# Performance work log

Hardware: AMD Instinct MI355X
Metric: run time of the kernel (lower is better)

## Reference

```python
import jax, jax.numpy as jnp
import numpy as np

B = 8
INPUT_SHAPE = (32, 32, 32)
N = int(np.prod(INPUT_SHAPE))  # 32768
K = 128


def setup_inputs() -> dict:
    key = jax.random.key(0)
    k1, k2, k3, k4 = jax.random.split(key, 4)
    data = jax.random.normal(k1, (B,) + INPUT_SHAPE, dtype=jnp.float32)
    mask = jax.random.uniform(k2, (B,) + INPUT_SHAPE, dtype=jnp.float32)
    mult = jax.random.normal(k3, (N, K), dtype=jnp.float32) * 0.05  # RandomNormal init
    sigma_sq = jax.random.normal(k4, (1,), dtype=jnp.float32) * 0.05
    return {"data": data, "mask": mask, "mult": mult, "sigma_sq": sigma_sq}


def reference(data, mask, mult, sigma_sq):
    # Two-arg branch of SpatiallySparseDense_old.call (a_fact == 1).
    b = data.shape[0]
    n, k = mult.shape
    data_flat = data.reshape(b, n)          # [B, N]
    mask_flat = mask.reshape(b, n)          # [B, N]
    # W0 = mask_flat * mult, per batch: [B, N, K]
    W0 = mask_flat[:, :, None] * mult[None, :, :]
    # Gram matrix W0^T W0 + sigma^2 * I : [B, K, K]
    gram = jnp.einsum('bnk,bnl->bkl', W0, W0)
    seye = sigma_sq[0] * jnp.eye(k, dtype=data.dtype)
    pre = jnp.linalg.inv(gram + seye[None])  # [B, K, K] (matches tf.linalg.inv)
    # m = W0^T data : [B, K, 1]
    m = jnp.einsum('bnk,bn->bk', W0, data_flat)[..., None]
    res = jnp.matmul(pre, m)                # [B, K, 1]
    return res
```

## Files before the change

### kernel.cpp

```cpp
#include <hip/hip_runtime.h>

#define BATCH 8
#define NN 32768
#define KK 128
#define NCHUNK 32
#define CHUNK 1024
#define NST 16
#define NITER 8

typedef __attribute__((ext_vector_type(8)))  _Float16 half8;
typedef __attribute__((ext_vector_type(4)))  _Float16 half4;
typedef __attribute__((ext_vector_type(16))) float    f32x16;

#define MT_OFF   0ull
#define WH_OFF   (MT_OFF + 8388608ull)
#define DH_OFF   (WH_OFF + 524288ull)
#define GP_OFF   (DH_OFF + 524288ull)
#define MP_OFF   (GP_OFF + 5242880ull)
#define G_OFF    (MP_OFF + 131072ull)

__global__ __launch_bounds__(256) void prep_kernel(
    const float* __restrict__ data, const float* __restrict__ mask,
    const float* __restrict__ mult, unsigned char* __restrict__ ws)
{
    __shared__ _Float16 t[128][136];
    const int tid = threadIdx.x;
    const int n0  = blockIdx.x * 128;

    {
        const int b = tid >> 5, q = tid & 31;
        const size_t src = (size_t)b * NN + n0 + q * 4;
        const float4 d4 = *(const float4*)(data + src);
        const float4 m4 = *(const float4*)(mask + src);
        half4 w = { (_Float16)m4.x, (_Float16)m4.y, (_Float16)m4.z, (_Float16)m4.w };
        half4 d = { (_Float16)d4.x, (_Float16)d4.y, (_Float16)d4.z, (_Float16)d4.w };
        *(half4*)((_Float16*)(ws + WH_OFF) + src) = w;
        *(half4*)((_Float16*)(ws + DH_OFF) + src) = d;
    }

    const float4* m4p = (const float4*)mult;
#pragma unroll
    for (int u = 0; u < 16; ++u) {
        const int c16 = u * 256 + tid;
        const int n  = c16 >> 5;
        const int kq = c16 & 31;
        float4 v = m4p[(size_t)(n0 + n) * 32 + kq];
        half4 h = { (_Float16)v.x, (_Float16)v.y, (_Float16)v.z, (_Float16)v.w };
        const int c4s = kq ^ ((n >> 3) & 7);
        *(half4*)&t[n][c4s * 4] = h;
    }
    __syncthreads();

    _Float16* mt = (_Float16*)(ws + MT_OFF);
    const int g = tid & 15;
#pragma unroll
    for (int i = 0; i < 8; ++i) {
        const int k = (tid >> 4) + i * 16;
        const int c4 = (k >> 2) ^ 7;
        half8 v;
#pragma unroll
        for (int j = 0; j < 8; ++j) {
            const int n = g * 8 + j;
            const int cs = (k >> 2) ^ ((n >> 3) & 7);
            v[j] = t[n][cs * 4 + (k & 3)];
        }
        (void)c4;
        *(half8*)(mt + (size_t)k * NN + n0 + g * 8) = v;
    }
}

__global__ __launch_bounds__(256, 1) void gram_kernel(
    unsigned char* __restrict__ ws)
{
    __shared__ unsigned char smem[36864];
    const int tid = threadIdx.x;
    const int b     = blockIdx.x >> 5;
    const int chunk = blockIdx.x & 31;
    const int n0    = chunk * CHUNK;
    const int w = tid >> 6, l = tid & 63;

    const _Float16* mt = (const _Float16*)(ws + MT_OFF);

    if (tid < 128) {
        half8 wv = *(const half8*)((const _Float16*)(ws + WH_OFF) + (size_t)b * NN + n0 + tid * 8);
        half8 dv = *(const half8*)((const _Float16*)(ws + DH_OFF) + (size_t)b * NN + n0 + tid * 8);
        *(half8*)(smem + 32768 + tid * 16) = wv;
        *(half8*)(smem + 34816 + tid * 16) = dv;
    }

    const int krow = tid >> 3;
    const int gd   = tid & 7;
    const _Float16* gsrc0 = mt + (size_t)krow * NN + n0 + gd * 8;
    const int wslot = (gd ^ (krow & 7)) * 16;

    uint4 S0, S1, S2, S3;
#define GLOAD(st_) { const _Float16* p = gsrc0 + (size_t)(st_) * 64;          \
        S0 = *(const uint4*)(p);                                              \
        S1 = *(const uint4*)(p + (size_t)32 * NN);                            \
        S2 = *(const uint4*)(p + (size_t)64 * NN);                            \
        S3 = *(const uint4*)(p + (size_t)96 * NN); }
#define DSWRITE(buf_) { unsigned char* bp = smem + (buf_) * 16384 + krow * 128 + wslot; \
        *(uint4*)(bp)         = S0;  *(uint4*)(bp + 4096)  = S1;              \
        *(uint4*)(bp + 8192)  = S2;  *(uint4*)(bp + 12288) = S3; }

    const int frow  = (l & 31) * 128;
    const int fslot = ((w * 2 + (l >> 5)) ^ (l & 7)) * 16;
    const int wdoff = w * 32 + (l >> 5) * 16;

    f32x16 a00 = {}, a01 = {}, a02 = {}, a03 = {}, a11 = {},
           a12 = {}, a13 = {}, a22 = {}, a23 = {}, a33 = {};
    float macc0 = 0.f, macc1 = 0.f, macc2 = 0.f, macc3 = 0.f;

    GLOAD(0);
    __syncthreads();
    DSWRITE(0);
    GLOAD(1);
    __syncthreads();

#pragma unroll 2
    for (int st = 0; st < NST; ++st) {
        const int cur = st & 1;
        if (st < NST - 1) {
            DSWRITE(cur ^ 1);
            if (st < NST - 2) GLOAD(st + 2);
        }
        const unsigned char* tb = smem + cur * 16384;
        const half8 wf = *(const half8*)(smem + 32768 + st * 128 + wdoff);
        const half8 df = *(const half8*)(smem + 34816 + st * 128 + wdoff);
        half8 f0 = *(const half8*)(tb +     0 + frow + fslot) * wf;
        half8 f1 = *(const half8*)(tb +  4096 + frow + fslot) * wf;
        half8 f2 = *(const half8*)(tb +  8192 + frow + fslot) * wf;
        half8 f3 = *(const half8*)(tb + 12288 + frow + fslot) * wf;
#pragma unroll
        for (int j = 0; j < 8; ++j) {
            const float dj = (float)df[j];
            macc0 = fmaf((float)f0[j], dj, macc0);
            macc1 = fmaf((float)f1[j], dj, macc1);
            macc2 = fmaf((float)f2[j], dj, macc2);
            macc3 = fmaf((float)f3[j], dj, macc3);
        }
        a00 = __builtin_amdgcn_mfma_f32_32x32x16_f16(f0, f0, a00, 0, 0, 0);
        a01 = __builtin_amdgcn_mfma_f32_32x32x16_f16(f0, f1, a01, 0, 0, 0);
        a02 = __builtin_amdgcn_mfma_f32_32x32x16_f16(f0, f2, a02, 0, 0, 0);
        a03 = __builtin_amdgcn_mfma_f32_32x32x16_f16(f0, f3, a03, 0, 0, 0);
        a11 = __builtin_amdgcn_mfma_f32_32x32x16_f16(f1, f1, a11, 0, 0, 0);
        a12 = __builtin_amdgcn_mfma_f32_32x32x16_f16(f1, f2, a12, 0, 0, 0);
        a13 = __builtin_amdgcn_mfma_f32_32x32x16_f16(f1, f3, a13, 0, 0, 0);
        a22 = __builtin_amdgcn_mfma_f32_32x32x16_f16(f2, f2, a22, 0, 0, 0);
        a23 = __builtin_amdgcn_mfma_f32_32x32x16_f16(f2, f3, a23, 0, 0, 0);
        a33 = __builtin_amdgcn_mfma_f32_32x32x16_f16(f3, f3, a33, 0, 0, 0);
        __syncthreads();
    }

    {
        float* M = (float*)(smem + 32768);
        const int base = (w * 2 + (l >> 5)) * 128 + (l & 31);
        M[base +  0] = macc0;  M[base + 32] = macc1;
        M[base + 64] = macc2;  M[base + 96] = macc3;
    }
    _Float16* Gp = (_Float16*)(ws + GP_OFF) + (size_t)(b * NCHUNK + chunk) * 10240;
    float* Mp = (float*)(ws + MP_OFF) + (size_t)(b * NCHUNK + chunk) * KK;
    float* R = (float*)smem;

#define PHASE(p_, A0_, A1_)                                                    \
    {                                                                          \
        *(f32x16*)(R + (w * 2 + 0) * 1024 + l * 16) = A0_;                     \
        *(f32x16*)(R + (w * 2 + 1) * 1024 + l * 16) = A1_;                     \
        __syncthreads();                                                       \
        _Pragma("unroll")                                                      \
        for (int pass = 0; pass < 2; ++pass) {                                 \
            const int e = pass * 1024 + tid * 4;                               \
            float4 s0 = *(float4*)(R + e);                                     \
            float4 s1 = *(float4*)(R + 2048 + e);                              \
            float4 s2 = *(float4*)(R + 4096 + e);                              \
            float4 s3 = *(float4*)(R + 6144 + e);                              \
            float sx = s0.x + s1.x + s2.x + s3.x;                              \
            float sy = s0.y + s1.y + s2.y + s3.y;                              \
            float sz = s0.z + s1.z + s2.z + s3.z;                              \
            float sw = s0.w + s1.w + s2.w + s3.w;                              \
            half4 h = { (_Float16)sx, (_Float16)sy, (_Float16)sz, (_Float16)sw }; \
            *(half4*)(Gp + (p_) * 2048 + e) = h;                               \
        }                                                                      \
        if ((p_) == 0 && tid < 128) {                                          \
            const float* M = (const float*)(smem + 32768);                     \
            float s = 0.f;                                                     \
            _Pragma("unroll")                                                  \
            for (int c8 = 0; c8 < 8; ++c8) s += M[c8 * 128 + tid];             \
            Mp[tid] = s;                                                       \
        }                                                                      \
        __syncthreads();                                                       \
    }

    PHASE(0, a00, a01)
    PHASE(1, a02, a03)
    PHASE(2, a11, a12)
    PHASE(3, a13, a22)
    PHASE(4, a23, a33)
#undef PHASE
#undef GLOAD
#undef DSWRITE
}

__global__ __launch_bounds__(256) void reduce_kernel(
    const float* __restrict__ sig, unsigned char* __restrict__ ws)
{
    const int tid = threadIdx.x;
    const int b  = blockIdx.x / 5;
    const int t2 = blockIdx.x % 5;

    const int e_local = tid * 8;
    const int tile = t2 * 2 + (e_local >> 10);
    const int off  = e_local & 1023;
    const int lane = off >> 4;
    const int r0   = off & 15;

    const _Float16* Gp = (const _Float16*)(ws + GP_OFF)
                       + (size_t)b * NCHUNK * 10240 + (size_t)t2 * 2048 + e_local;
    float s[8] = {0.f,0.f,0.f,0.f,0.f,0.f,0.f,0.f};
#pragma unroll
    for (int ch = 0; ch < NCHUNK; ++ch) {
        half8 v = *(const half8*)(Gp + (size_t)ch * 10240);
#pragma unroll
        for (int j = 0; j < 8; ++j) s[j] += (float)v[j];
    }

    static const int TT[10] = {0,0,0,0,1,1,1,2,2,3};
    static const int UU[10] = {0,1,2,3,1,2,3,2,3,3};
    const int tt = TT[tile], uu = UU[tile];
    const int C = uu * 32 + (lane & 31);
    float* G = (float*)(ws + G_OFF) + (size_t)b * 16384;
    const float sg = sig[0];
#pragma unroll
    for (int j = 0; j < 8; ++j) {
        const int reg = r0 + j;
        const int row = (reg & 3) + 8 * (reg >> 2) + 4 * (lane >> 5);
        const int Rr = tt * 32 + row;
        float v = s[j];
        G[Rr * KK + C] = (Rr == C) ? v + sg : v;
        if (tt != uu) G[C * KK + Rr] = v;
    }
}

__device__ __forceinline__ float blockDot(float a, float bvl, float* red)
{
    float v = a * bvl;
#pragma unroll
    for (int off = 32; off > 0; off >>= 1) v += __shfl_down(v, off, 64);
    const int wid = threadIdx.x >> 6;
    if ((threadIdx.x & 63) == 0) red[wid] = v;
    __syncthreads();
    float s = red[0] + red[1];
    __syncthreads();
    return s;
}

__global__ __launch_bounds__(128, 1) void solve_kernel(
    const unsigned char* __restrict__ ws, float* __restrict__ out)
{
    const int b = blockIdx.x;
    const int i = threadIdx.x;

    __shared__ float ps[KK];
    __shared__ float red[2];

    const float* G  = (const float*)(ws + G_OFF) + (size_t)b * 16384;
    const float* Mp = (const float*)(ws + MP_OFF) + (size_t)b * NCHUNK * KK;

    float Gr[KK];
#pragma unroll
    for (int j = 0; j < KK; ++j) Gr[j] = G[j * KK + i];

    float mvv = 0.f;
#pragma unroll
    for (int ch = 0; ch < NCHUNK; ++ch) mvv += Mp[ch * KK + i];

    float x = 0.f, r = mvv, p = r;
    ps[i] = p;
    float rs = blockDot(r, r, red);

    for (int it = 0; it < NITER; ++it) {
        float q0 = 0.f, q1 = 0.f, q2 = 0.f, q3 = 0.f;
#pragma unroll
        for (int u = 0; u < 32; ++u) {
            float4 pv = *reinterpret_cast<const float4*>(&ps[4 * u]);
            q0 = fmaf(Gr[4 * u + 0], pv.x, q0);
            q1 = fmaf(Gr[4 * u + 1], pv.y, q1);
            q2 = fmaf(Gr[4 * u + 2], pv.z, q2);
            q3 = fmaf(Gr[4 * u + 3], pv.w, q3);
        }
        float q = (q0 + q1) + (q2 + q3);

        float pq    = blockDot(p, q, red);
        float alpha = rs / (pq + 1e-30f);
        x = fmaf(alpha, p, x);
        r = fmaf(-alpha, q, r);
        float rs2  = blockDot(r, r, red);
        float beta = rs2 / (rs + 1e-30f);
        rs = rs2;
        p  = fmaf(beta, p, r);
        ps[i] = p;
        __syncthreads();
    }
    out[(size_t)b * KK + i] = x;
}

extern "C" void kernel_launch(void* const* d_in, const int* in_sizes, int n_in,
                              void* d_out, int out_size, void* d_ws, size_t ws_size,
                              hipStream_t stream)
{
    const float* data = (const float*)d_in[0];
    const float* mask = (const float*)d_in[1];
    const float* mult = (const float*)d_in[2];
    const float* sig  = (const float*)d_in[3];
    unsigned char* ws = (unsigned char*)d_ws;
    float* out = (float*)d_out;

    prep_kernel  <<<256, 256, 0, stream>>>(data, mask, mult, ws);
    gram_kernel  <<<BATCH * NCHUNK, 256, 0, stream>>>(ws);
    reduce_kernel<<<BATCH * 5, 256, 0, stream>>>(sig, ws);
    solve_kernel <<<BATCH, 128, 0, stream>>>(ws, out);
}
```

Measured before the change: 103.1 us.

## Fuse Gram partial reduction into solve kernel and split matvec across two halves

Removes the separate reduce kernel. The solve kernel now sums the per-chunk fp16 Gram partials itself, builds the full 128x128 matrix in shared memory with sigma added on the diagonal, and uses 256 threads. Each half of the block holds 64 rows of G in registers and the two partial matvec results are combined through shared memory. This saves one launch and a global round trip of G, and halves per-thread register pressure. In exchange, the partial reduction now runs on only 8 blocks instead of 40, and each CG iteration gains extra barriers.

```diff
diff --git a/kernel.cpp b/kernel.cpp
--- a/kernel.cpp
+++ b/kernel.cpp
@@ -17,7 +17,6 @@
 #define DH_OFF   (WH_OFF + 524288ull)
 #define GP_OFF   (DH_OFF + 524288ull)
 #define MP_OFF   (GP_OFF + 5242880ull)
-#define G_OFF    (MP_OFF + 131072ull)
 
 __global__ __launch_bounds__(256) void prep_kernel(
     const float* __restrict__ data, const float* __restrict__ mask,
@@ -56,7 +55,6 @@
 #pragma unroll
     for (int i = 0; i < 8; ++i) {
         const int k = (tid >> 4) + i * 16;
-        const int c4 = (k >> 2) ^ 7;
         half8 v;
 #pragma unroll
         for (int j = 0; j < 8; ++j) {
@@ -64,7 +62,6 @@
             const int cs = (k >> 2) ^ ((n >> 3) & 7);
             v[j] = t[n][cs * 4 + (k & 3)];
         }
-        (void)c4;
         *(half8*)(mt + (size_t)k * NN + n0 + g * 8) = v;
     }
 }
@@ -201,47 +198,7 @@
 #undef DSWRITE
 }
 
-__global__ __launch_bounds__(256) void reduce_kernel(
-    const float* __restrict__ sig, unsigned char* __restrict__ ws)
-{
-    const int tid = threadIdx.x;
-    const int b  = blockIdx.x / 5;
-    const int t2 = blockIdx.x % 5;
-
-    const int e_local = tid * 8;
-    const int tile = t2 * 2 + (e_local >> 10);
-    const int off  = e_local & 1023;
-    const int lane = off >> 4;
-    const int r0   = off & 15;
-
-    const _Float16* Gp = (const _Float16*)(ws + GP_OFF)
-                       + (size_t)b * NCHUNK * 10240 + (size_t)t2 * 2048 + e_local;
-    float s[8] = {0.f,0.f,0.f,0.f,0.f,0.f,0.f,0.f};
-#pragma unroll
-    for (int ch = 0; ch < NCHUNK; ++ch) {
-        half8 v = *(const half8*)(Gp + (size_t)ch * 10240);
-#pragma unroll
-        for (int j = 0; j < 8; ++j) s[j] += (float)v[j];
-    }
-
-    static const int TT[10] = {0,0,0,0,1,1,1,2,2,3};
-    static const int UU[10] = {0,1,2,3,1,2,3,2,3,3};
-    const int tt = TT[tile], uu = UU[tile];
-    const int C = uu * 32 + (lane & 31);
-    float* G = (float*)(ws + G_OFF) + (size_t)b * 16384;
-    const float sg = sig[0];
-#pragma unroll
-    for (int j = 0; j < 8; ++j) {
-        const int reg = r0 + j;
-        const int row = (reg & 3) + 8 * (reg >> 2) + 4 * (lane >> 5);
-        const int Rr = tt * 32 + row;
-        float v = s[j];
-        G[Rr * KK + C] = (Rr == C) ? v + sg : v;
-        if (tt != uu) G[C * KK + Rr] = v;
-    }
-}
-
-__device__ __forceinline__ float blockDot(float a, float bvl, float* red)
+__device__ __forceinline__ float blockDot4(float a, float bvl, float* red)
 {
     float v = a * bvl;
 #pragma unroll
@@ -249,59 +206,101 @@
     const int wid = threadIdx.x >> 6;
     if ((threadIdx.x & 63) == 0) red[wid] = v;
     __syncthreads();
-    float s = red[0] + red[1];
+    float s = (red[0] + red[1]) + (red[2] + red[3]);
     __syncthreads();
     return s;
 }
 
-__global__ __launch_bounds__(128, 1) void solve_kernel(
-    const unsigned char* __restrict__ ws, float* __restrict__ out)
-{
-    const int b = blockIdx.x;
-    const int i = threadIdx.x;
-
+__global__ __launch_bounds__(256, 1) void solve_kernel(
+    const float* __restrict__ sig, const unsigned char* __restrict__ ws,
+    float* __restrict__ out)
+{
+    __shared__ float Gl[KK * KK];
     __shared__ float ps[KK];
-    __shared__ float red[2];
-
-    const float* G  = (const float*)(ws + G_OFF) + (size_t)b * 16384;
+    __shared__ float qex[256];
+    __shared__ float red[4];
+
+    const int tid = threadIdx.x;
+    const int b   = blockIdx.x;
+    const int i   = tid & 127;
+    const int h   = tid >> 7;
+
+    static const int TT[10] = {0,0,0,0,1,1,1,2,2,3};
+    static const int UU[10] = {0,1,2,3,1,2,3,2,3,3};
+    const _Float16* Gp = (const _Float16*)(ws + GP_OFF) + (size_t)b * NCHUNK * 10240;
+    const float sg = sig[0];
+    const int lane = i >> 1;
+    const int r0   = (i & 1) * 8;
+    const int C0   = lane & 31;
+    const int rhi  = 4 * (lane >> 5);
+
+#pragma unroll
+    for (int gi = 0; gi < 5; ++gi) {
+        const int e = (gi * 256 + tid) * 8;
+        float s[8] = {0.f,0.f,0.f,0.f,0.f,0.f,0.f,0.f};
+        const _Float16* gp = Gp + e;
+#pragma unroll
+        for (int ch = 0; ch < NCHUNK; ++ch) {
+            half8 v = *(const half8*)(gp + (size_t)ch * 10240);
+#pragma unroll
+            for (int j = 0; j < 8; ++j) s[j] += (float)v[j];
+        }
+        const int tile = gi * 2 + h;
+        const int tt = TT[tile], uu = UU[tile];
+        const int C = uu * 32 + C0;
+#pragma unroll
+        for (int j = 0; j < 8; ++j) {
+            const int reg = r0 + j;
+            const int row = (reg & 3) + 8 * (reg >> 2) + rhi;
+            const int Rr = tt * 32 + row;
+            const float v = s[j];
+            Gl[Rr * KK + C] = (Rr == C) ? v + sg : v;
+            if (tt != uu) Gl[C * KK + Rr] = v;
+        }
+    }
+    __syncthreads();
+
+    float Gr[64];
+#pragma unroll
+    for (int j = 0; j < 64; ++j) Gr[j] = Gl[(h * 64 + j) * KK + i];
+
     const float* Mp = (const float*)(ws + MP_OFF) + (size_t)b * NCHUNK * KK;
-
-    float Gr[KK];
-#pragma unroll
-    for (int j = 0; j < KK; ++j) Gr[j] = G[j * KK + i];
-
     float mvv = 0.f;
 #pragma unroll
     for (int ch = 0; ch < NCHUNK; ++ch) mvv += Mp[ch * KK + i];
 
     float x = 0.f, r = mvv, p = r;
     ps[i] = p;
-    float rs = blockDot(r, r, red);
+    float rs = blockDot4(r, r, red);
 
     for (int it = 0; it < NITER; ++it) {
         float q0 = 0.f, q1 = 0.f, q2 = 0.f, q3 = 0.f;
-#pragma unroll
-        for (int u = 0; u < 32; ++u) {
-            float4 pv = *reinterpret_cast<const float4*>(&ps[4 * u]);
+        const float* psh = ps + h * 64;
+#pragma unroll
+        for (int u = 0; u < 16; ++u) {
+            float4 pv = *(const float4*)(psh + 4 * u);
             q0 = fmaf(Gr[4 * u + 0], pv.x, q0);
             q1 = fmaf(Gr[4 * u + 1], pv.y, q1);
             q2 = fmaf(Gr[4 * u + 2], pv.z, q2);
             q3 = fmaf(Gr[4 * u + 3], pv.w, q3);
         }
-        float q = (q0 + q1) + (q2 + q3);
-
-        float pq    = blockDot(p, q, red);
+        qex[tid] = (q0 + q1) + (q2 + q3);
+        __syncthreads();
+        const float q = qex[i] + qex[128 + i];
+
+        float pq    = blockDot4(p, q, red);
         float alpha = rs / (pq + 1e-30f);
         x = fmaf(alpha, p, x);
         r = fmaf(-alpha, q, r);
-        float rs2  = blockDot(r, r, red);
+        float rs2  = blockDot4(r, r, red);
         float beta = rs2 / (rs + 1e-30f);
         rs = rs2;
         p  = fmaf(beta, p, r);
+        __syncthreads();
         ps[i] = p;
         __syncthreads();
     }
-    out[(size_t)b * KK + i] = x;
+    if (h == 0) out[(size_t)b * KK + i] = x;
 }
 
 extern "C" void kernel_launch(void* const* d_in, const int* in_sizes, int n_in,
@@ -315,8 +314,7 @@
     unsigned char* ws = (unsigned char*)d_ws;
     float* out = (float*)d_out;
 
-    prep_kernel  <<<256, 256, 0, stream>>>(data, mask, mult, ws);
-    gram_kernel  <<<BATCH * NCHUNK, 256, 0, stream>>>(ws);
-    reduce_kernel<<<BATCH * 5, 256, 0, stream>>>(sig, ws);
-    solve_kernel <<<BATCH, 128, 0, stream>>>(ws, out);
-}
+    prep_kernel <<<256, 256, 0, stream>>>(data, mask, mult, ws);
+    gram_kernel <<<BATCH * NCHUNK, 256, 0, stream>>>(ws);
+    solve_kernel<<<BATCH, 256, 0, stream>>>(sig, ws, out);
+}
```

New measurement: 109.0 us. +5.7%, slower.
